# Kernel optimization log

Measured on AMD Instinct MI355X. Metric: run time of the kernel, lower is better.

Reference implementation:

```python
import jax, jax.numpy as jnp
import numpy as np

VOCAB, E, H = 32000, 256, 256
B, T = 64, 2048


def setup_inputs() -> dict:
    key = jax.random.key(0)
    ks = jax.random.split(key, 6)
    X = jax.random.randint(ks[0], (B, T), 0, VOCAB)
    emb = jax.random.normal(ks[1], (VOCAB, E), dtype=jnp.float32)
    W_qrnn = jax.random.normal(ks[2], (E, 3 * H), dtype=jnp.float32) / np.sqrt(E)
    b_qrnn = jnp.zeros((3 * H,), dtype=jnp.float32)
    c0 = jax.random.normal(ks[3], (B, H), dtype=jnp.float32)
    W_out = jax.random.normal(ks[4], (H, 1), dtype=jnp.float32) / np.sqrt(H)
    b_out = jnp.zeros((1,), dtype=jnp.float32)
    return {"X": X, "emb": emb, "W_qrnn": W_qrnn, "b_qrnn": b_qrnn,
            "c0": c0, "W_out": W_out, "b_out": b_out}


def reference(X, emb, W_qrnn, b_qrnn, c0, W_out, b_out):
    # Embedding lookup: [B,T] -> [B,T,E]; permute to seq-major [T,B,E]
    x = jnp.transpose(emb[X], (1, 0, 2))
    # QRNN window=1 gate projection: all timesteps in one GEMM, [T,B,3H]
    g = jnp.einsum('tbe,ef->tbf', x, W_qrnn) + b_qrnn
    z, f, o = jnp.split(g, 3, axis=-1)
    z = jnp.tanh(z)
    f = jax.nn.sigmoid(f)
    o = jax.nn.sigmoid(o)

    # fo-pooling recurrence: c_t = f_t * c_{t-1} + (1 - f_t) * z_t
    def step(c, zf):
        z_t, f_t = zf
        c = f_t * c + (1.0 - f_t) * z_t
        return c, c

    _, cs = jax.lax.scan(step, c0, (z, f))  # cs: [T,B,H]
    h = o * cs                              # h_t = o_t * c_t
    hn = h[-1]                              # last timestep, [B,H]
    return hn @ W_out + b_out               # [B,1]
```

## Files before the change

### kernel.cpp

```cpp
#include <hip/hip_runtime.h>
#include <hip/hip_bf16.h>
#include <math.h>

#define EDIM 256
#define HDIM 256
#define BDIM 64
#define TDIM 2048
#define NC   64
#define TC   32
#define CPB  4

typedef __attribute__((ext_vector_type(8)))  short  short8;
typedef __attribute__((ext_vector_type(4)))  float  floatx4;
typedef __attribute__((ext_vector_type(4)))  unsigned int uintx4;

__device__ __forceinline__ unsigned short f2bf(float f) {
    unsigned int u = __float_as_uint(f);
    u += 0x7FFFu + ((u >> 16) & 1u);
    return (unsigned short)(u >> 16);
}
__device__ __forceinline__ unsigned int pk2(float a, float b) {
    return (unsigned int)f2bf(a) | ((unsigned int)f2bf(b) << 16);
}
__device__ __forceinline__ float sigm(float x) {
    return __builtin_amdgcn_rcpf(1.f + __expf(-x));
}
__device__ __forceinline__ float tanh_fast(float x) {
    return fmaf(-2.f, __builtin_amdgcn_rcpf(1.f + __expf(2.f * x)), 1.f);
}

__global__ __launch_bounds__(256) void qrnn_pack(
    const float* __restrict__ Wq, const float* __restrict__ emb,
    unsigned short* __restrict__ Wp, unsigned short* __restrict__ ebf)
{
    const int bx = blockIdx.x;
    if (bx < 256) {
        const int nt = (bx >> 3) & 7;
        const int hg = bx >> 6;
        const int ks = bx & 7;
        const int t = threadIdx.x;
        const int lane = t >> 2, pj = t & 3;
        const int col = lane & 15, q = lane >> 4;
        const int h = hg * 64 + (nt & 3) * 16 + col;
        const int c = (nt < 4) ? h : (HDIM + h);
        const int k = ks * 32 + q * 8 + pj * 2;
        unsigned int v = pk2(Wq[k * (3 * HDIM) + c], Wq[(k + 1) * (3 * HDIM) + c]);
        *(unsigned int*)(Wp + (size_t)bx * 512 + lane * 8 + pj * 2) = v;
    } else {
        size_t i = ((size_t)(bx - 256) * 256 + threadIdx.x) * 8;
        floatx4 a = *(const floatx4*)(emb + i);
        floatx4 b = *(const floatx4*)(emb + i + 4);
        uintx4 o = {pk2(a.x, a.y), pk2(a.z, a.w), pk2(b.x, b.y), pk2(b.z, b.w)};
        *(uintx4*)(ebf + i) = o;
    }
}

template<bool EMBBF>
__global__ __launch_bounds__(256, 2) void qrnn_mfma(
    const int* __restrict__ X, const float* __restrict__ emb,
    const unsigned short* __restrict__ ebf, const unsigned short* __restrict__ Wp,
    const float* __restrict__ bq, float* __restrict__ wsA, float* __restrict__ wsB)
{
    __shared__ __align__(16) short Bsh[32768];

    const int tid = threadIdx.x;
    const int cg = blockIdx.x, bg = blockIdx.y, hg = blockIdx.z;
    const int lane = tid & 63, w = tid >> 6;
    const int col = lane & 15, q = lane >> 4;

    const unsigned short* wpb = Wp + (size_t)hg * 32768;
#pragma unroll
    for (int i = 0; i < 16; ++i) {
        const int ch = w * 16 + i;
        __builtin_amdgcn_global_load_lds(
            (const __attribute__((address_space(1))) unsigned int*)(wpb + ch * 512 + lane * 8),
            (__attribute__((address_space(3))) unsigned int*)(Bsh + ch * 512),
            16, 0, 0);
    }

    const int b0 = bg * 8 + 2 * w;
    int xid[CPB][4];
#pragma unroll
    for (int c = 0; c < CPB; ++c)
#pragma unroll
        for (int mt = 0; mt < 4; ++mt)
            xid[c][mt] = X[(b0 + (mt >> 1)) * TDIM + (cg * CPB + c) * TC + (mt & 1) * 16 + col];

    const int hbase = hg * 64;
    float bz[4], bff[4];
#pragma unroll
    for (int nt = 0; nt < 4; ++nt) {
        bz[nt]  = bq[hbase + nt * 16 + col];
        bff[nt] = bq[HDIM + hbase + nt * 16 + col];
    }

    short8 abuf[3][4];
    auto fetchA = [&](int c, int ks, int slot) {
#pragma unroll
        for (int mt = 0; mt < 4; ++mt) {
            if constexpr (EMBBF) {
                abuf[slot][mt] = *(const short8*)(ebf + (size_t)xid[c][mt] * EDIM + q * 8 + ks * 32);
            } else {
                const float* ap = emb + (size_t)xid[c][mt] * EDIM + q * 8 + ks * 32;
                floatx4 f0 = *(const floatx4*)ap;
                floatx4 f1 = *(const floatx4*)(ap + 4);
                uintx4 p = {pk2(f0.x, f0.y), pk2(f0.z, f0.w),
                            pk2(f1.x, f1.y), pk2(f1.z, f1.w)};
                abuf[slot][mt] = *(short8*)&p;
            }
        }
    };

    floatx4 acc[4][8];
#pragma unroll
    for (int mt = 0; mt < 4; ++mt)
#pragma unroll
        for (int nt = 0; nt < 8; ++nt) acc[mt][nt] = (floatx4){0.f, 0.f, 0.f, 0.f};

    fetchA(0, 0, 0);
    fetchA(0, 1, 1);
    __syncthreads();

#pragma unroll
    for (int c = 0; c < CPB; ++c) {
#pragma unroll
        for (int ks = 0; ks < 8; ++ks) {
            const int s = c * 8 + ks;
            if (s + 2 < CPB * 8)
                fetchA((s + 2) >> 3, (s + 2) & 7, (s + 2) % 3);
            short8 bf[8];
#pragma unroll
            for (int nt = 0; nt < 8; ++nt)
                bf[nt] = *(const short8*)(Bsh + (nt * 8 + ks) * 512 + lane * 8);
            const int sl = s % 3;
#pragma unroll
            for (int nt = 0; nt < 8; ++nt)
#pragma unroll
                for (int mt = 0; mt < 4; ++mt)
                    acc[mt][nt] = __builtin_amdgcn_mfma_f32_16x16x32_bf16(abuf[sl][mt], bf[nt], acc[mt][nt], 0, 0, 0);
        }

        const int cc = cg * CPB + c;
        float Af0[4], Bf0[4], Af1[4], Bf1[4];
#pragma unroll
        for (int nt = 0; nt < 4; ++nt) {
            float Aseg[4], Bseg[4];
#pragma unroll
            for (int mt = 0; mt < 4; ++mt) {
                float Ac = 1.f, Bc = 0.f;
#pragma unroll
                for (int j = 0; j < 4; ++j) {
                    float z = tanh_fast(acc[mt][nt][j] + bz[nt]);
                    float f = sigm(acc[mt][nt + 4][j] + bff[nt]);
                    Ac = f * Ac;
                    Bc = fmaf(f, Bc, (1.f - f) * z);
                }
                Aseg[mt] = Ac; Bseg[mt] = Bc;
            }
#pragma unroll
            for (int st = 0; st < 2; ++st) {
                const int msk = 16 << st;
                const bool self_earlier = ((q >> st) & 1) == 0;
#pragma unroll
                for (int mt = 0; mt < 4; ++mt) {
                    float Ap = __shfl_xor(Aseg[mt], msk, 64);
                    float Bp = __shfl_xor(Bseg[mt], msk, 64);
                    Bseg[mt] = self_earlier ? fmaf(Ap, Bseg[mt], Bp)
                                            : fmaf(Aseg[mt], Bp, Bseg[mt]);
                    Aseg[mt] = Aseg[mt] * Ap;
                }
            }
            Af0[nt] = Aseg[0] * Aseg[1];
            Bf0[nt] = fmaf(Aseg[1], Bseg[0], Bseg[1]);
            Af1[nt] = Aseg[2] * Aseg[3];
            Bf1[nt] = fmaf(Aseg[3], Bseg[2], Bseg[3]);
        }

        float As0 = (q == 0) ? Af0[0] : (q == 1) ? Af0[1] : (q == 2) ? Af0[2] : Af0[3];
        float Bs0 = (q == 0) ? Bf0[0] : (q == 1) ? Bf0[1] : (q == 2) ? Bf0[2] : Bf0[3];
        float As1 = (q == 0) ? Af1[0] : (q == 1) ? Af1[1] : (q == 2) ? Af1[2] : Af1[3];
        float Bs1 = (q == 0) ? Bf1[0] : (q == 1) ? Bf1[1] : (q == 2) ? Bf1[2] : Bf1[3];

        const size_t r0 = ((size_t)cc * BDIM + b0) * HDIM + hbase + lane;
        wsA[r0] = As0;          wsB[r0] = Bs0;
        wsA[r0 + HDIM] = As1;   wsB[r0 + HDIM] = Bs1;

#pragma unroll
        for (int mt = 0; mt < 4; ++mt)
#pragma unroll
            for (int nt = 0; nt < 8; ++nt) acc[mt][nt] = (floatx4){0.f, 0.f, 0.f, 0.f};
    }
}

__global__ __launch_bounds__(256) void qrnn_combine(
    const float* __restrict__ wsA, const float* __restrict__ wsB,
    const float* __restrict__ c0, const int* __restrict__ X,
    const float* __restrict__ emb, const float* __restrict__ Wq,
    const float* __restrict__ bq, const float* __restrict__ Wout,
    const float* __restrict__ bout, float* __restrict__ out)
{
    const int b = blockIdx.x;
    const int h = threadIdx.x;

    float c = c0[b * HDIM + h];
    for (int c8 = 0; c8 < NC; c8 += 8) {
        float a[8], bb[8];
#pragma unroll
        for (int i = 0; i < 8; ++i) {
            size_t base = ((size_t)(c8 + i) * BDIM + b) * HDIM + h;
            a[i]  = wsA[base];
            bb[i] = wsB[base];
        }
#pragma unroll
        for (int i = 0; i < 8; ++i) c = fmaf(a[i], c, bb[i]);
    }

    __shared__ float xs[EDIM];
    int idx = X[b * TDIM + (TDIM - 1)];
    xs[h] = emb[(size_t)idx * EDIM + h];
    __syncthreads();

    float acc = 0.f;
#pragma unroll 16
    for (int e = 0; e < EDIM; ++e)
        acc = fmaf(xs[e], Wq[e * (3 * HDIM) + 2 * HDIM + h], acc);

    float o  = 1.f / (1.f + expf(-(acc + bq[2 * HDIM + h])));
    float hn = o * c;

    __shared__ float red[HDIM];
    red[h] = hn * Wout[h];
    __syncthreads();
    for (int s = HDIM / 2; s > 0; s >>= 1) {
        if (h < s) red[h] += red[h + s];
        __syncthreads();
    }
    if (h == 0) out[b] = red[0] + bout[0];
}

extern "C" void kernel_launch(void* const* d_in, const int* in_sizes, int n_in,
                              void* d_out, int out_size, void* d_ws, size_t ws_size,
                              hipStream_t stream) {
    const int*   X    = (const int*)d_in[0];
    const float* emb  = (const float*)d_in[1];
    const float* Wq   = (const float*)d_in[2];
    const float* bq   = (const float*)d_in[3];
    const float* c0   = (const float*)d_in[4];
    const float* Wout = (const float*)d_in[5];
    const float* bout = (const float*)d_in[6];
    float* out = (float*)d_out;

    float* wsA = (float*)d_ws;
    float* wsB = wsA + (size_t)NC * BDIM * HDIM;
    unsigned short* Wp  = (unsigned short*)(wsB + (size_t)NC * BDIM * HDIM);
    unsigned short* ebf = Wp + (size_t)256 * 512;

    const size_t need_full = (size_t)2 * NC * BDIM * HDIM * 4
                           + (size_t)256 * 512 * 2
                           + (size_t)32000 * EDIM * 2;
    const bool full = ws_size >= need_full;

    const int emb_blocks = (32000 * EDIM / 8) / 256;
    qrnn_pack<<<256 + (full ? emb_blocks : 0), 256, 0, stream>>>(Wq, emb, Wp, ebf);

    dim3 g(NC / CPB, BDIM / 8, HDIM / 64);
    if (full) qrnn_mfma<true ><<<g, 256, 0, stream>>>(X, emb, ebf, Wp, bq, wsA, wsB);
    else      qrnn_mfma<false><<<g, 256, 0, stream>>>(X, emb, ebf, Wp, bq, wsA, wsB);

    qrnn_combine<<<BDIM, 256, 0, stream>>>(wsA, wsB, c0, X, emb, Wq, bq, Wout, bout, out);
}
```

Measured before the change: 150.0 us.

## Fuse pack, MFMA gate scan and combine into one cooperative kernel

```diff
diff --git a/kernel.cpp b/kernel.cpp
--- a/kernel.cpp
+++ b/kernel.cpp
@@ -1,6 +1,9 @@
 #include <hip/hip_runtime.h>
 #include <hip/hip_bf16.h>
+#include <hip/hip_cooperative_groups.h>
 #include <math.h>
+
+namespace cg = cooperative_groups;
 
 #define EDIM 256
 #define HDIM 256
@@ -29,42 +32,240 @@
     return fmaf(-2.f, __builtin_amdgcn_rcpf(1.f + __expf(2.f * x)), 1.f);
 }
 
-__global__ __launch_bounds__(256) void qrnn_pack(
-    const float* __restrict__ Wq, const float* __restrict__ emb,
-    unsigned short* __restrict__ Wp, unsigned short* __restrict__ ebf)
+__global__ __launch_bounds__(256, 2) void qrnn_fused(
+    const int* __restrict__ X, const float* __restrict__ emb,
+    unsigned short* __restrict__ ebf, unsigned short* __restrict__ Wp,
+    const float* __restrict__ bq, const float* __restrict__ c0,
+    const float* __restrict__ Wq, const float* __restrict__ Wout,
+    const float* __restrict__ bout, float* __restrict__ wsA,
+    float* __restrict__ wsB, float* __restrict__ out)
 {
-    const int bx = blockIdx.x;
+    __shared__ __align__(16) short Bsh[32768];
+    cg::grid_group grid = cg::this_grid();
+
+    const int tid = threadIdx.x;
+    const int bx  = blockIdx.x;
+    const int lane = tid & 63, w = tid >> 6;
+    const int col = lane & 15, q = lane >> 4;
+
     if (bx < 256) {
         const int nt = (bx >> 3) & 7;
         const int hg = bx >> 6;
         const int ks = bx & 7;
-        const int t = threadIdx.x;
-        const int lane = t >> 2, pj = t & 3;
-        const int col = lane & 15, q = lane >> 4;
-        const int h = hg * 64 + (nt & 3) * 16 + col;
+        const int plane = tid >> 2, pj = tid & 3;
+        const int pcol = plane & 15, pq = plane >> 4;
+        const int h = hg * 64 + (nt & 3) * 16 + pcol;
         const int c = (nt < 4) ? h : (HDIM + h);
-        const int k = ks * 32 + q * 8 + pj * 2;
+        const int k = ks * 32 + pq * 8 + pj * 2;
         unsigned int v = pk2(Wq[k * (3 * HDIM) + c], Wq[(k + 1) * (3 * HDIM) + c]);
-        *(unsigned int*)(Wp + (size_t)bx * 512 + lane * 8 + pj * 2) = v;
-    } else {
-        size_t i = ((size_t)(bx - 256) * 256 + threadIdx.x) * 8;
-        floatx4 a = *(const floatx4*)(emb + i);
-        floatx4 b = *(const floatx4*)(emb + i + 4);
-        uintx4 o = {pk2(a.x, a.y), pk2(a.z, a.w), pk2(b.x, b.y), pk2(b.z, b.w)};
-        *(uintx4*)(ebf + i) = o;
-    }
-}
-
-template<bool EMBBF>
-__global__ __launch_bounds__(256, 2) void qrnn_mfma(
+        *(unsigned int*)(Wp + (size_t)bx * 512 + plane * 8 + pj * 2) = v;
+    }
+#pragma unroll
+    for (int it = 0; it < 8; ++it) {
+        int gidx = it * 131072 + bx * 256 + tid;
+        if (gidx < 1024000) {
+            size_t i = (size_t)gidx * 8;
+            floatx4 a = *(const floatx4*)(emb + i);
+            floatx4 b = *(const floatx4*)(emb + i + 4);
+            uintx4 o = {pk2(a.x, a.y), pk2(a.z, a.w), pk2(b.x, b.y), pk2(b.z, b.w)};
+            *(uintx4*)(ebf + i) = o;
+        }
+    }
+
+    __threadfence();
+    grid.sync();
+
+    {
+        const int cgi = bx & 15, bg = (bx >> 4) & 7, hg = bx >> 7;
+
+        const unsigned short* wpb = Wp + (size_t)hg * 32768;
+#pragma unroll
+        for (int i = 0; i < 16; ++i) {
+            const int ch = w * 16 + i;
+            __builtin_amdgcn_global_load_lds(
+                (const __attribute__((address_space(1))) unsigned int*)(wpb + ch * 512 + lane * 8),
+                (__attribute__((address_space(3))) unsigned int*)(Bsh + ch * 512),
+                16, 0, 0);
+        }
+
+        const int b0 = bg * 8 + 2 * w;
+        int xid[CPB][4];
+#pragma unroll
+        for (int c = 0; c < CPB; ++c)
+#pragma unroll
+            for (int mt = 0; mt < 4; ++mt)
+                xid[c][mt] = X[(b0 + (mt >> 1)) * TDIM + (cgi * CPB + c) * TC + (mt & 1) * 16 + col];
+
+        const int hbase = hg * 64;
+        float bz[4], bff[4];
+#pragma unroll
+        for (int nt = 0; nt < 4; ++nt) {
+            bz[nt]  = bq[hbase + nt * 16 + col];
+            bff[nt] = bq[HDIM + hbase + nt * 16 + col];
+        }
+
+        short8 abuf[4][4];
+        auto fetchA = [&](int c, int ks, int slot) {
+#pragma unroll
+            for (int mt = 0; mt < 4; ++mt)
+                abuf[slot][mt] = *(const short8*)(ebf + (size_t)xid[c][mt] * EDIM + q * 8 + ks * 32);
+        };
+
+        floatx4 acc[4][8];
+#pragma unroll
+        for (int mt = 0; mt < 4; ++mt)
+#pragma unroll
+            for (int nt = 0; nt < 8; ++nt) acc[mt][nt] = (floatx4){0.f, 0.f, 0.f, 0.f};
+
+        fetchA(0, 0, 0);
+        fetchA(0, 1, 1);
+        fetchA(0, 2, 2);
+        __syncthreads();
+
+#pragma unroll
+        for (int c = 0; c < CPB; ++c) {
+#pragma unroll
+            for (int ks = 0; ks < 8; ++ks) {
+                const int s = c * 8 + ks;
+                if (s + 3 < CPB * 8)
+                    fetchA((s + 3) >> 3, (s + 3) & 7, (s + 3) & 3);
+                const int sl = s & 3;
+#pragma unroll
+                for (int nh = 0; nh < 2; ++nh) {
+                    short8 bf[4];
+#pragma unroll
+                    for (int j = 0; j < 4; ++j)
+                        bf[j] = *(const short8*)(Bsh + ((nh * 4 + j) * 8 + ks) * 512 + lane * 8);
+#pragma unroll
+                    for (int j = 0; j < 4; ++j)
+#pragma unroll
+                        for (int mt = 0; mt < 4; ++mt)
+                            acc[mt][nh * 4 + j] = __builtin_amdgcn_mfma_f32_16x16x32_bf16(
+                                abuf[sl][mt], bf[j], acc[mt][nh * 4 + j], 0, 0, 0);
+                }
+            }
+
+            const int cc = cgi * CPB + c;
+            float Af0[4], Bf0[4], Af1[4], Bf1[4];
+#pragma unroll
+            for (int nt = 0; nt < 4; ++nt) {
+                float Aseg[4], Bseg[4];
+#pragma unroll
+                for (int mt = 0; mt < 4; ++mt) {
+                    float Ac = 1.f, Bc = 0.f;
+#pragma unroll
+                    for (int j = 0; j < 4; ++j) {
+                        float z = tanh_fast(acc[mt][nt][j] + bz[nt]);
+                        float f = sigm(acc[mt][nt + 4][j] + bff[nt]);
+                        Ac = f * Ac;
+                        Bc = fmaf(f, Bc, (1.f - f) * z);
+                    }
+                    Aseg[mt] = Ac; Bseg[mt] = Bc;
+                }
+#pragma unroll
+                for (int st = 0; st < 2; ++st) {
+                    const int msk = 16 << st;
+                    const bool self_earlier = ((q >> st) & 1) == 0;
+#pragma unroll
+                    for (int mt = 0; mt < 4; ++mt) {
+                        float Ap = __shfl_xor(Aseg[mt], msk, 64);
+                        float Bp = __shfl_xor(Bseg[mt], msk, 64);
+                        Bseg[mt] = self_earlier ? fmaf(Ap, Bseg[mt], Bp)
+                                                : fmaf(Aseg[mt], Bp, Bseg[mt]);
+                        Aseg[mt] = Aseg[mt] * Ap;
+                    }
+                }
+                Af0[nt] = Aseg[0] * Aseg[1];
+                Bf0[nt] = fmaf(Aseg[1], Bseg[0], Bseg[1]);
+                Af1[nt] = Aseg[2] * Aseg[3];
+                Bf1[nt] = fmaf(Aseg[3], Bseg[2], Bseg[3]);
+            }
+
+            float As0 = (q == 0) ? Af0[0] : (q == 1) ? Af0[1] : (q == 2) ? Af0[2] : Af0[3];
+            float Bs0 = (q == 0) ? Bf0[0] : (q == 1) ? Bf0[1] : (q == 2) ? Bf0[2] : Bf0[3];
+            float As1 = (q == 0) ? Af1[0] : (q == 1) ? Af1[1] : (q == 2) ? Af1[2] : Af1[3];
+            float Bs1 = (q == 0) ? Bf1[0] : (q == 1) ? Bf1[1] : (q == 2) ? Bf1[2] : Bf1[3];
+
+            const size_t r0 = ((size_t)cc * BDIM + b0) * HDIM + hbase + lane;
+            wsA[r0] = As0;          wsB[r0] = Bs0;
+            wsA[r0 + HDIM] = As1;   wsB[r0 + HDIM] = Bs1;
+
+#pragma unroll
+            for (int mt = 0; mt < 4; ++mt)
+#pragma unroll
+                for (int nt = 0; nt < 8; ++nt) acc[mt][nt] = (floatx4){0.f, 0.f, 0.f, 0.f};
+        }
+    }
+
+    __threadfence();
+    grid.sync();
+
+    if (bx < BDIM) {
+        const int b = bx;
+        const int h = tid;
+
+        float c = c0[b * HDIM + h];
+        for (int c8 = 0; c8 < NC; c8 += 8) {
+            float a[8], bb[8];
+#pragma unroll
+            for (int i = 0; i < 8; ++i) {
+                size_t base = ((size_t)(c8 + i) * BDIM + b) * HDIM + h;
+                a[i]  = wsA[base];
+                bb[i] = wsB[base];
+            }
+#pragma unroll
+            for (int i = 0; i < 8; ++i) c = fmaf(a[i], c, bb[i]);
+        }
+
+        float* xs  = (float*)Bsh;
+        float* red = xs + EDIM;
+        int idx = X[b * TDIM + (TDIM - 1)];
+        xs[h] = emb[(size_t)idx * EDIM + h];
+        __syncthreads();
+
+        float acc2 = 0.f;
+#pragma unroll 16
+        for (int e = 0; e < EDIM; ++e)
+            acc2 = fmaf(xs[e], Wq[e * (3 * HDIM) + 2 * HDIM + h], acc2);
+
+        float o  = 1.f / (1.f + expf(-(acc2 + bq[2 * HDIM + h])));
+        float hn = o * c;
+
+        red[h] = hn * Wout[h];
+        __syncthreads();
+        for (int s = HDIM / 2; s > 0; s >>= 1) {
+            if (h < s) red[h] += red[h + s];
+            __syncthreads();
+        }
+        if (h == 0) out[b] = red[0] + bout[0];
+    }
+}
+
+__global__ __launch_bounds__(256) void qrnn_pack_fb(
+    const float* __restrict__ Wq, unsigned short* __restrict__ Wp)
+{
+    const int bx = blockIdx.x;
+    const int nt = (bx >> 3) & 7;
+    const int hg = bx >> 6;
+    const int ks = bx & 7;
+    const int t = threadIdx.x;
+    const int lane = t >> 2, pj = t & 3;
+    const int col = lane & 15, q = lane >> 4;
+    const int h = hg * 64 + (nt & 3) * 16 + col;
+    const int c = (nt < 4) ? h : (HDIM + h);
+    const int k = ks * 32 + q * 8 + pj * 2;
+    unsigned int v = pk2(Wq[k * (3 * HDIM) + c], Wq[(k + 1) * (3 * HDIM) + c]);
+    *(unsigned int*)(Wp + (size_t)bx * 512 + lane * 8 + pj * 2) = v;
+}
+
+__global__ __launch_bounds__(256, 2) void qrnn_mfma_fb(
     const int* __restrict__ X, const float* __restrict__ emb,
-    const unsigned short* __restrict__ ebf, const unsigned short* __restrict__ Wp,
-    const float* __restrict__ bq, float* __restrict__ wsA, float* __restrict__ wsB)
+    const unsigned short* __restrict__ Wp, const float* __restrict__ bq,
+    float* __restrict__ wsA, float* __restrict__ wsB)
 {
     __shared__ __align__(16) short Bsh[32768];
-
     const int tid = threadIdx.x;
-    const int cg = blockIdx.x, bg = blockIdx.y, hg = blockIdx.z;
+    const int cgi = blockIdx.x, bg = blockIdx.y, hg = blockIdx.z;
     const int lane = tid & 63, w = tid >> 6;
     const int col = lane & 15, q = lane >> 4;
 
@@ -84,7 +285,7 @@
     for (int c = 0; c < CPB; ++c)
 #pragma unroll
         for (int mt = 0; mt < 4; ++mt)
-            xid[c][mt] = X[(b0 + (mt >> 1)) * TDIM + (cg * CPB + c) * TC + (mt & 1) * 16 + col];
+            xid[c][mt] = X[(b0 + (mt >> 1)) * TDIM + (cgi * CPB + c) * TC + (mt & 1) * 16 + col];
 
     const int hbase = hg * 64;
     float bz[4], bff[4];
@@ -94,20 +295,16 @@
         bff[nt] = bq[HDIM + hbase + nt * 16 + col];
     }
 
-    short8 abuf[3][4];
+    short8 abuf[4][4];
     auto fetchA = [&](int c, int ks, int slot) {
 #pragma unroll
         for (int mt = 0; mt < 4; ++mt) {
-            if constexpr (EMBBF) {
-                abuf[slot][mt] = *(const short8*)(ebf + (size_t)xid[c][mt] * EDIM + q * 8 + ks * 32);
-            } else {
-                const float* ap = emb + (size_t)xid[c][mt] * EDIM + q * 8 + ks * 32;
-                floatx4 f0 = *(const floatx4*)ap;
-                floatx4 f1 = *(const floatx4*)(ap + 4);
-                uintx4 p = {pk2(f0.x, f0.y), pk2(f0.z, f0.w),
-                            pk2(f1.x, f1.y), pk2(f1.z, f1.w)};
-                abuf[slot][mt] = *(short8*)&p;
-            }
+            const float* ap = emb + (size_t)xid[c][mt] * EDIM + q * 8 + ks * 32;
+            floatx4 f0 = *(const floatx4*)ap;
+            floatx4 f1 = *(const floatx4*)(ap + 4);
+            uintx4 p = {pk2(f0.x, f0.y), pk2(f0.z, f0.w),
+                        pk2(f1.x, f1.y), pk2(f1.z, f1.w)};
+            abuf[slot][mt] = *(short8*)&p;
         }
     };
 
@@ -119,6 +316,7 @@
 
     fetchA(0, 0, 0);
     fetchA(0, 1, 1);
+    fetchA(0, 2, 2);
     __syncthreads();
 
 #pragma unroll
@@ -126,21 +324,25 @@
 #pragma unroll
         for (int ks = 0; ks < 8; ++ks) {
             const int s = c * 8 + ks;
-            if (s + 2 < CPB * 8)
-                fetchA((s + 2) >> 3, (s + 2) & 7, (s + 2) % 3);
-            short8 bf[8];
-#pragma unroll
-            for (int nt = 0; nt < 8; ++nt)
-                bf[nt] = *(const short8*)(Bsh + (nt * 8 + ks) * 512 + lane * 8);
-            const int sl = s % 3;
-#pragma unroll
-            for (int nt = 0; nt < 8; ++nt)
-#pragma unroll
-                for (int mt = 0; mt < 4; ++mt)
-                    acc[mt][nt] = __builtin_amdgcn_mfma_f32_16x16x32_bf16(abuf[sl][mt], bf[nt], acc[mt][nt], 0, 0, 0);
-        }
-
-        const int cc = cg * CPB + c;
+            if (s + 3 < CPB * 8)
+                fetchA((s + 3) >> 3, (s + 3) & 7, (s + 3) & 3);
+            const int sl = s & 3;
+#pragma unroll
+            for (int nh = 0; nh < 2; ++nh) {
+                short8 bf[4];
+#pragma unroll
+                for (int j = 0; j < 4; ++j)
+                    bf[j] = *(const short8*)(Bsh + ((nh * 4 + j) * 8 + ks) * 512 + lane * 8);
+#pragma unroll
+                for (int j = 0; j < 4; ++j)
+#pragma unroll
+                    for (int mt = 0; mt < 4; ++mt)
+                        acc[mt][nh * 4 + j] = __builtin_amdgcn_mfma_f32_16x16x32_bf16(
+                            abuf[sl][mt], bf[j], acc[mt][nh * 4 + j], 0, 0, 0);
+            }
+        }
+
+        const int cc = cgi * CPB + c;
         float Af0[4], Bf0[4], Af1[4], Bf1[4];
 #pragma unroll
         for (int nt = 0; nt < 4; ++nt) {
@@ -192,7 +394,7 @@
     }
 }
 
-__global__ __launch_bounds__(256) void qrnn_combine(
+__global__ __launch_bounds__(256) void qrnn_combine_fb(
     const float* __restrict__ wsA, const float* __restrict__ wsB,
     const float* __restrict__ c0, const int* __restrict__ X,
     const float* __restrict__ emb, const float* __restrict__ Wq,
@@ -260,12 +462,21 @@
                            + (size_t)32000 * EDIM * 2;
     const bool full = ws_size >= need_full;
 
-    const int emb_blocks = (32000 * EDIM / 8) / 256;
-    qrnn_pack<<<256 + (full ? emb_blocks : 0), 256, 0, stream>>>(Wq, emb, Wp, ebf);
-
-    dim3 g(NC / CPB, BDIM / 8, HDIM / 64);
-    if (full) qrnn_mfma<true ><<<g, 256, 0, stream>>>(X, emb, ebf, Wp, bq, wsA, wsB);
-    else      qrnn_mfma<false><<<g, 256, 0, stream>>>(X, emb, ebf, Wp, bq, wsA, wsB);
-
-    qrnn_combine<<<BDIM, 256, 0, stream>>>(wsA, wsB, c0, X, emb, Wq, bq, Wout, bout, out);
-}
+    bool done = false;
+    if (full) {
+        void* args[] = {(void*)&X, (void*)&emb, (void*)&ebf, (void*)&Wp,
+                        (void*)&bq, (void*)&c0, (void*)&Wq, (void*)&Wout,
+                        (void*)&bout, (void*)&wsA, (void*)&wsB, (void*)&out};
+        hipError_t e = hipLaunchCooperativeKernel(
+            reinterpret_cast<void*>(qrnn_fused), dim3(512), dim3(256),
+            args, 0, stream);
+        done = (e == hipSuccess);
+    }
+
+    if (!done) {
+        qrnn_pack_fb<<<256, 256, 0, stream>>>(Wq, Wp);
+        dim3 g(NC / CPB, BDIM / 8, HDIM / 64);
+        qrnn_mfma_fb<<<g, 256, 0, stream>>>(X, emb, Wp, bq, wsA, wsB);
+        qrnn_combine_fb<<<BDIM, 256, 0, stream>>>(wsA, wsB, c0, X, emb, Wq, bq, Wout, bout, out);
+    }
+}
```

Result: slower. 375.1 us (+150.1%).

## Drop separate pack kernel; pack weights into LDS inside the MFMA kernel

Applied to the files above, without the earlier changes.

```diff
diff --git a/kernel.cpp b/kernel.cpp
--- a/kernel.cpp
+++ b/kernel.cpp
@@ -29,53 +29,31 @@
     return fmaf(-2.f, __builtin_amdgcn_rcpf(1.f + __expf(2.f * x)), 1.f);
 }
 
-__global__ __launch_bounds__(256) void qrnn_pack(
-    const float* __restrict__ Wq, const float* __restrict__ emb,
-    unsigned short* __restrict__ Wp, unsigned short* __restrict__ ebf)
-{
-    const int bx = blockIdx.x;
-    if (bx < 256) {
-        const int nt = (bx >> 3) & 7;
-        const int hg = bx >> 6;
-        const int ks = bx & 7;
-        const int t = threadIdx.x;
-        const int lane = t >> 2, pj = t & 3;
-        const int col = lane & 15, q = lane >> 4;
-        const int h = hg * 64 + (nt & 3) * 16 + col;
-        const int c = (nt < 4) ? h : (HDIM + h);
-        const int k = ks * 32 + q * 8 + pj * 2;
-        unsigned int v = pk2(Wq[k * (3 * HDIM) + c], Wq[(k + 1) * (3 * HDIM) + c]);
-        *(unsigned int*)(Wp + (size_t)bx * 512 + lane * 8 + pj * 2) = v;
-    } else {
-        size_t i = ((size_t)(bx - 256) * 256 + threadIdx.x) * 8;
-        floatx4 a = *(const floatx4*)(emb + i);
-        floatx4 b = *(const floatx4*)(emb + i + 4);
-        uintx4 o = {pk2(a.x, a.y), pk2(a.z, a.w), pk2(b.x, b.y), pk2(b.z, b.w)};
-        *(uintx4*)(ebf + i) = o;
-    }
-}
-
-template<bool EMBBF>
 __global__ __launch_bounds__(256, 2) void qrnn_mfma(
     const int* __restrict__ X, const float* __restrict__ emb,
-    const unsigned short* __restrict__ ebf, const unsigned short* __restrict__ Wp,
-    const float* __restrict__ bq, float* __restrict__ wsA, float* __restrict__ wsB)
+    const float* __restrict__ Wq, const float* __restrict__ bq,
+    float* __restrict__ wsA, float* __restrict__ wsB)
 {
     __shared__ __align__(16) short Bsh[32768];
 
     const int tid = threadIdx.x;
-    const int cg = blockIdx.x, bg = blockIdx.y, hg = blockIdx.z;
+    const int cgi = blockIdx.x, bg = blockIdx.y, hg = blockIdx.z;
     const int lane = tid & 63, w = tid >> 6;
     const int col = lane & 15, q = lane >> 4;
-
-    const unsigned short* wpb = Wp + (size_t)hg * 32768;
-#pragma unroll
-    for (int i = 0; i < 16; ++i) {
-        const int ch = w * 16 + i;
-        __builtin_amdgcn_global_load_lds(
-            (const __attribute__((address_space(1))) unsigned int*)(wpb + ch * 512 + lane * 8),
-            (__attribute__((address_space(3))) unsigned int*)(Bsh + ch * 512),
-            16, 0, 0);
+    const int hbase = hg * 64;
+
+    {
+        const int plane = tid >> 2, pj = tid & 3;
+        const int pcol = plane & 15, pq = plane >> 4;
+#pragma unroll 4
+        for (int sb = 0; sb < 64; ++sb) {
+            const int nt = sb >> 3, ks = sb & 7;
+            const int h = hbase + (nt & 3) * 16 + pcol;
+            const int c = (nt < 4) ? h : (HDIM + h);
+            const int k = ks * 32 + pq * 8 + pj * 2;
+            unsigned int v = pk2(Wq[k * (3 * HDIM) + c], Wq[(k + 1) * (3 * HDIM) + c]);
+            *(unsigned int*)(Bsh + sb * 512 + plane * 8 + pj * 2) = v;
+        }
     }
 
     const int b0 = bg * 8 + 2 * w;
@@ -84,9 +62,8 @@
     for (int c = 0; c < CPB; ++c)
 #pragma unroll
         for (int mt = 0; mt < 4; ++mt)
-            xid[c][mt] = X[(b0 + (mt >> 1)) * TDIM + (cg * CPB + c) * TC + (mt & 1) * 16 + col];
-
-    const int hbase = hg * 64;
+            xid[c][mt] = X[(b0 + (mt >> 1)) * TDIM + (cgi * CPB + c) * TC + (mt & 1) * 16 + col];
+
     float bz[4], bff[4];
 #pragma unroll
     for (int nt = 0; nt < 4; ++nt) {
@@ -98,16 +75,12 @@
     auto fetchA = [&](int c, int ks, int slot) {
 #pragma unroll
         for (int mt = 0; mt < 4; ++mt) {
-            if constexpr (EMBBF) {
-                abuf[slot][mt] = *(const short8*)(ebf + (size_t)xid[c][mt] * EDIM + q * 8 + ks * 32);
-            } else {
-                const float* ap = emb + (size_t)xid[c][mt] * EDIM + q * 8 + ks * 32;
-                floatx4 f0 = *(const floatx4*)ap;
-                floatx4 f1 = *(const floatx4*)(ap + 4);
-                uintx4 p = {pk2(f0.x, f0.y), pk2(f0.z, f0.w),
-                            pk2(f1.x, f1.y), pk2(f1.z, f1.w)};
-                abuf[slot][mt] = *(short8*)&p;
-            }
+            const float* ap = emb + (size_t)xid[c][mt] * EDIM + q * 8 + ks * 32;
+            floatx4 f0 = *(const floatx4*)ap;
+            floatx4 f1 = *(const floatx4*)(ap + 4);
+            uintx4 p = {pk2(f0.x, f0.y), pk2(f0.z, f0.w),
+                        pk2(f1.x, f1.y), pk2(f1.z, f1.w)};
+            abuf[slot][mt] = *(short8*)&p;
         }
     };
 
@@ -128,19 +101,23 @@
             const int s = c * 8 + ks;
             if (s + 2 < CPB * 8)
                 fetchA((s + 2) >> 3, (s + 2) & 7, (s + 2) % 3);
-            short8 bf[8];
-#pragma unroll
-            for (int nt = 0; nt < 8; ++nt)
-                bf[nt] = *(const short8*)(Bsh + (nt * 8 + ks) * 512 + lane * 8);
             const int sl = s % 3;
 #pragma unroll
-            for (int nt = 0; nt < 8; ++nt)
-#pragma unroll
-                for (int mt = 0; mt < 4; ++mt)
-                    acc[mt][nt] = __builtin_amdgcn_mfma_f32_16x16x32_bf16(abuf[sl][mt], bf[nt], acc[mt][nt], 0, 0, 0);
-        }
-
-        const int cc = cg * CPB + c;
+            for (int nh = 0; nh < 2; ++nh) {
+                short8 bf[4];
+#pragma unroll
+                for (int j = 0; j < 4; ++j)
+                    bf[j] = *(const short8*)(Bsh + ((nh * 4 + j) * 8 + ks) * 512 + lane * 8);
+#pragma unroll
+                for (int j = 0; j < 4; ++j)
+#pragma unroll
+                    for (int mt = 0; mt < 4; ++mt)
+                        acc[mt][nh * 4 + j] = __builtin_amdgcn_mfma_f32_16x16x32_bf16(
+                            abuf[sl][mt], bf[j], acc[mt][nh * 4 + j], 0, 0, 0);
+            }
+        }
+
+        const int cc = cgi * CPB + c;
         float Af0[4], Bf0[4], Af1[4], Bf1[4];
 #pragma unroll
         for (int nt = 0; nt < 4; ++nt) {
@@ -252,20 +229,8 @@
 
     float* wsA = (float*)d_ws;
     float* wsB = wsA + (size_t)NC * BDIM * HDIM;
-    unsigned short* Wp  = (unsigned short*)(wsB + (size_t)NC * BDIM * HDIM);
-    unsigned short* ebf = Wp + (size_t)256 * 512;
-
-    const size_t need_full = (size_t)2 * NC * BDIM * HDIM * 4
-                           + (size_t)256 * 512 * 2
-                           + (size_t)32000 * EDIM * 2;
-    const bool full = ws_size >= need_full;
-
-    const int emb_blocks = (32000 * EDIM / 8) / 256;
-    qrnn_pack<<<256 + (full ? emb_blocks : 0), 256, 0, stream>>>(Wq, emb, Wp, ebf);
 
     dim3 g(NC / CPB, BDIM / 8, HDIM / 64);
-    if (full) qrnn_mfma<true ><<<g, 256, 0, stream>>>(X, emb, ebf, Wp, bq, wsA, wsB);
-    else      qrnn_mfma<false><<<g, 256, 0, stream>>>(X, emb, ebf, Wp, bq, wsA, wsB);
-
+    qrnn_mfma<<<g, 256, 0, stream>>>(X, emb, Wq, bq, wsA, wsB);
     qrnn_combine<<<BDIM, 256, 0, stream>>>(wsA, wsB, c0, X, emb, Wq, bq, Wout, bout, out);
 }
```

Measured after the change: 267.4 us. 78.3% more time.
